# Kernel optimization log

Measured on AMD Instinct MI355X. Metric: run time of the kernel, lower is better.

## Reference

```python
import jax, jax.numpy as jnp
import numpy as np

N_IN = 50000
N_OUT = 50000
DEG = 16
E = N_OUT * DEG
C = 64
F = 64


def cartesian_to_spherical(cart, extents):
    # cart: [E,3]
    r_plane_2 = cart[..., 0] ** 2 + cart[..., 1] ** 2
    r_2 = r_plane_2 + cart[..., 2] ** 2
    r_safe = jnp.maximum(jnp.sqrt(r_2), 1e-10)
    cos_phi = cart[..., 2] / r_safe
    r_plane_safe = jnp.maximum(jnp.sqrt(r_plane_2), 1e-10)
    sin_theta = cart[..., 1] / r_plane_safe
    cos_theta = cart[..., 0] / r_plane_safe
    r_normalized = r_safe / extents
    return jnp.stack([r_normalized, cos_phi, sin_theta, cos_theta], axis=-1)  # [E,4]


def setup_inputs() -> dict:
    key = jax.random.key(0)
    k1, k2, k3, k4, k5 = jax.random.split(key, 5)
    input_features = jax.random.normal(k1, (N_IN, C), dtype=jnp.float32)
    input_positions = jax.random.uniform(k2, (N_IN, 3), dtype=jnp.float32)
    output_positions = jax.random.uniform(k3, (N_OUT, 3), dtype=jnp.float32)
    extents = jnp.ones((1,), dtype=jnp.float32)
    kernel = jax.random.normal(k4, (4, C, F), dtype=jnp.float32) * (1.0 / np.sqrt(C))
    bias = jnp.zeros((F,), dtype=jnp.float32)
    neighbors_index = jax.random.randint(k5, (E,), 0, N_IN, dtype=jnp.int32)
    neighbors_row_splits = (DEG * jnp.arange(N_OUT + 1)).astype(jnp.int32)
    return {
        "input_features": input_features,
        "input_positions": input_positions,
        "output_positions": output_positions,
        "extents": extents,
        "kernel": kernel,
        "bias": bias,
        "neighbors_index": neighbors_index,
        "neighbors_row_splits": neighbors_row_splits,
    }


def reference(input_features, input_positions, output_positions, extents,
              kernel, bias, neighbors_index, neighbors_row_splits):
    n_out = output_positions.shape[0]
    n_edges = neighbors_index.shape[0]
    counts = neighbors_row_splits[1:] - neighbors_row_splits[:-1]  # [N_out]
    # segment id of each edge (which output point it belongs to)
    seg_ids = jnp.repeat(jnp.arange(n_out), counts, total_repeat_length=n_edges)
    expanded_query = output_positions[seg_ids]                     # [E,3]
    difference = input_positions[neighbors_index] - expanded_query  # [E,3]
    sph = cartesian_to_spherical(difference, extents)              # [E,4]
    neighbors_feats = input_features[neighbors_index]              # [E,C]
    # contract features with kernel over C first -> [E,4,F] (avoids [E,C,F])
    tmp = jnp.einsum('ec,scf->esf', neighbors_feats, kernel)
    out_edge = jnp.einsum('es,esf->ef', sph, tmp)                  # [E,F]
    out_features = jax.ops.segment_sum(out_edge, seg_ids, num_segments=n_out)
    out_features = out_features + bias
    return out_features
```

## Files before the change

kernel.cpp:

```cpp
#include <hip/hip_runtime.h>

typedef unsigned short u16;
typedef __attribute__((ext_vector_type(8))) short bf16x8;
typedef __attribute__((ext_vector_type(4))) float f32x4;

#define WPB   4
#define BLOCK (WPB * 64)

__device__ __forceinline__ u16 f2bf(float f) {
    union { float f; unsigned u; } v; v.f = f;
    unsigned r = v.u + 0x7fff + ((v.u >> 16) & 1);
    return (u16)(r >> 16);
}

__global__ __launch_bounds__(BLOCK, 3)
void sphconv_mfma(const float* __restrict__ feats,
                  const float* __restrict__ in_pos,
                  const float* __restrict__ out_pos,
                  const float* __restrict__ extents,
                  const float* __restrict__ kmat,
                  const float* __restrict__ bias,
                  const int* __restrict__ nidx,
                  const int* __restrict__ rsplits,
                  float* __restrict__ out,
                  int n_out, int ntiles)
{
    __shared__ u16 KB[4 * 8 * 64 * 8];
    __shared__ int   idxL[WPB][16][16];
    __shared__ float sphL[WPB][16][16][4];

    const int tid  = threadIdx.x;
    const int wave = tid >> 6;
    const int lane = tid & 63;

    for (int i = tid; i < 16384; i += BLOCK) {
        const int n = i & 63, k = i >> 6;
        const int kstep = k >> 5, quad = (k >> 3) & 3, j = k & 7;
        const int ntile = n >> 4, lanep = (quad << 4) | (n & 15);
        KB[((((ntile << 3) | kstep) << 6) | lanep) * 8 + j] = f2bf(kmat[i]);
    }
    __syncthreads();

    const int tile = blockIdx.x * WPB + wave;
    if (tile >= ntiles) return;

    const float inv_ext = __fdividef(1.0f, extents[0]);

    #pragma unroll
    for (int u = 0; u < 4; ++u) {
        const int slot = (u << 6) | lane;
        const int m = slot >> 4, t = slot & 15;
        const int o = (tile << 4) | m;
        float rn = 0.f, cph = 0.f, sth = 0.f, cth = 0.f;
        int idx = 0;
        if (o < n_out) {
            const int e0 = rsplits[o], e1 = rsplits[o + 1];
            const int e = e0 + t;
            if (e < e1) {
                idx = nidx[e];
                const float dx = in_pos[idx * 3 + 0] - out_pos[o * 3 + 0];
                const float dy = in_pos[idx * 3 + 1] - out_pos[o * 3 + 1];
                const float dz = in_pos[idx * 3 + 2] - out_pos[o * 3 + 2];
                const float rp2 = dx * dx + dy * dy;
                const float r2  = rp2 + dz * dz;
                const float rs  = fmaxf(sqrtf(r2), 1e-10f);
                const float rp  = fmaxf(sqrtf(rp2), 1e-10f);
                const float ir  = __fdividef(1.0f, rs);
                const float irp = __fdividef(1.0f, rp);
                rn  = rs * inv_ext;
                cph = dz * ir;
                sth = dy * irp;
                cth = dx * irp;
            }
        }
        idxL[wave][t][m] = idx;
        f32x4 sv; sv.x = rn; sv.y = cph; sv.z = sth; sv.w = cth;
        *(f32x4*)&sphL[wave][t][m][0] = sv;
    }
    __builtin_amdgcn_wave_barrier();

    const int m    = lane & 15;
    const int quad = lane >> 4;
    float acc[8][8];
    #pragma unroll
    for (int ks = 0; ks < 8; ++ks)
        #pragma unroll
        for (int j = 0; j < 8; ++j) acc[ks][j] = 0.f;

    #pragma unroll 4
    for (int t = 0; t < 16; ++t) {
        const int   idx = idxL[wave][t][m];
        const f32x4 sv  = *(const f32x4*)&sphL[wave][t][m][0];
        const float* fr = feats + (idx << 6) + (quad << 3);
        const float4 lo0 = *(const float4*)(fr +  0);
        const float4 lo1 = *(const float4*)(fr +  4);
        const float4 hi0 = *(const float4*)(fr + 32);
        const float4 hi1 = *(const float4*)(fr + 36);
        #pragma unroll
        for (int s = 0; s < 4; ++s) {
            const float w = sv[s];
            float* aL = acc[2 * s];
            float* aH = acc[2 * s + 1];
            aL[0] = fmaf(w, lo0.x, aL[0]); aL[1] = fmaf(w, lo0.y, aL[1]);
            aL[2] = fmaf(w, lo0.z, aL[2]); aL[3] = fmaf(w, lo0.w, aL[3]);
            aL[4] = fmaf(w, lo1.x, aL[4]); aL[5] = fmaf(w, lo1.y, aL[5]);
            aL[6] = fmaf(w, lo1.z, aL[6]); aL[7] = fmaf(w, lo1.w, aL[7]);
            aH[0] = fmaf(w, hi0.x, aH[0]); aH[1] = fmaf(w, hi0.y, aH[1]);
            aH[2] = fmaf(w, hi0.z, aH[2]); aH[3] = fmaf(w, hi0.w, aH[3]);
            aH[4] = fmaf(w, hi1.x, aH[4]); aH[5] = fmaf(w, hi1.y, aH[5]);
            aH[6] = fmaf(w, hi1.z, aH[6]); aH[7] = fmaf(w, hi1.w, aH[7]);
        }
    }

    bf16x8 afr[8];
    #pragma unroll
    for (int ks = 0; ks < 8; ++ks) {
        union { u16 h[8]; bf16x8 v; } p;
        #pragma unroll
        for (int j = 0; j < 8; ++j) p.h[j] = f2bf(acc[ks][j]);
        afr[ks] = p.v;
    }

    const int obase = tile << 4;
    #pragma unroll
    for (int nt = 0; nt < 4; ++nt) {
        f32x4 C = {0.f, 0.f, 0.f, 0.f};
        const u16* kb = &KB[((nt << 3) << 6) * 8 + lane * 8];
        #pragma unroll
        for (int ks = 0; ks < 8; ++ks) {
            const bf16x8 b = *(const bf16x8*)(kb + (ks << 6) * 8);
            C = __builtin_amdgcn_mfma_f32_16x16x32_bf16(afr[ks], b, C, 0, 0, 0);
        }
        const int f  = (nt << 4) | m;
        const float bv = bias[f];
        #pragma unroll
        for (int r = 0; r < 4; ++r) {
            const int oo = obase + (quad << 2) + r;
            if (oo < n_out) out[(oo << 6) | f] = C[r] + bv;
        }
    }
}

extern "C" void kernel_launch(void* const* d_in, const int* in_sizes, int n_in,
                              void* d_out, int out_size, void* d_ws, size_t ws_size,
                              hipStream_t stream) {
    const float* feats   = (const float*)d_in[0];
    const float* in_pos  = (const float*)d_in[1];
    const float* out_pos = (const float*)d_in[2];
    const float* extents = (const float*)d_in[3];
    const float* kmat    = (const float*)d_in[4];
    const float* bias    = (const float*)d_in[5];
    const int*   nidx    = (const int*)d_in[6];
    const int*   rsplits = (const int*)d_in[7];
    const int n_out  = in_sizes[7] - 1;
    const int ntiles = (n_out + 15) >> 4;
    const int grid   = (ntiles + WPB - 1) / WPB;

    sphconv_mfma<<<grid, BLOCK, 0, stream>>>(
        feats, in_pos, out_pos, extents, kmat, bias, nidx, rsplits,
        (float*)d_out, n_out, ntiles);
}
```

Before: 128.3 us.

## Pre-convert features to bf16 in workspace and restructure gather with shuffles

Adds a prep kernel that converts the input features to bf16 and pre-swizzles the weight matrix into a workspace buffer. The main kernel then gathers half-size feature rows and copies the pre-swizzled weights instead of converting them per block. Spherical coordinates and neighbor indices now move through wave shuffles instead of LDS, and the channel dimension is processed in two halves to cut register pressure. The extra prep pass reads and writes the whole feature array each call and lowers the precision of the gathered features; a path without bf16 conversion is kept for when the workspace is too small.

```diff
diff --git a/kernel.cpp b/kernel.cpp
--- a/kernel.cpp
+++ b/kernel.cpp
@@ -2,141 +2,173 @@
 
 typedef unsigned short u16;
 typedef __attribute__((ext_vector_type(8))) short bf16x8;
+typedef __attribute__((ext_vector_type(8))) unsigned short u16x8;
 typedef __attribute__((ext_vector_type(4))) float f32x4;
 
 #define WPB   4
 #define BLOCK (WPB * 64)
 
+__device__ __forceinline__ float bf2f(u16 u) {
+    union { unsigned i; float f; } v; v.i = (unsigned)u << 16; return v.f;
+}
 __device__ __forceinline__ u16 f2bf(float f) {
     union { float f; unsigned u; } v; v.f = f;
     unsigned r = v.u + 0x7fff + ((v.u >> 16) & 1);
     return (u16)(r >> 16);
 }
 
+__global__ __launch_bounds__(256)
+void prep_kernel(const float* __restrict__ feats, const float* __restrict__ kmat,
+                 u16* __restrict__ fbf, u16* __restrict__ kbg, int nfeat8) {
+    const int id = blockIdx.x * 256 + threadIdx.x;
+    if (id < nfeat8) {
+        const float4 a = ((const float4*)feats)[2 * id];
+        const float4 b = ((const float4*)feats)[2 * id + 1];
+        union { u16 h[8]; int4 v; } p;
+        p.h[0] = f2bf(a.x); p.h[1] = f2bf(a.y); p.h[2] = f2bf(a.z); p.h[3] = f2bf(a.w);
+        p.h[4] = f2bf(b.x); p.h[5] = f2bf(b.y); p.h[6] = f2bf(b.z); p.h[7] = f2bf(b.w);
+        ((int4*)fbf)[id] = p.v;
+    }
+    if (id < 16384) {
+        const int k = id >> 6, n = id & 63;
+        const int nt = n >> 4, ks = k >> 5;
+        const int lanep = (((k >> 3) & 3) << 4) | (n & 15), j = k & 7;
+        kbg[(((((nt << 3) | ks) << 6) | lanep) << 3) | j] = f2bf(kmat[id]);
+    }
+}
+
+template<bool USE_WS>
 __global__ __launch_bounds__(BLOCK, 3)
-void sphconv_mfma(const float* __restrict__ feats,
-                  const float* __restrict__ in_pos,
-                  const float* __restrict__ out_pos,
-                  const float* __restrict__ extents,
-                  const float* __restrict__ kmat,
-                  const float* __restrict__ bias,
-                  const int* __restrict__ nidx,
-                  const int* __restrict__ rsplits,
-                  float* __restrict__ out,
-                  int n_out, int ntiles)
+void sphconv_main(const float* __restrict__ featsf, const u16* __restrict__ fbf,
+                  const float* __restrict__ in_pos, const float* __restrict__ out_pos,
+                  const float* __restrict__ extents, const float* __restrict__ kmat,
+                  const u16* __restrict__ kbg, const float* __restrict__ bias,
+                  const int* __restrict__ nidx, const int* __restrict__ rsplits,
+                  float* __restrict__ out, int n_out, int ntiles, int n_edges)
 {
-    __shared__ u16 KB[4 * 8 * 64 * 8];
-    __shared__ int   idxL[WPB][16][16];
-    __shared__ float sphL[WPB][16][16][4];
-
-    const int tid  = threadIdx.x;
-    const int wave = tid >> 6;
-    const int lane = tid & 63;
-
-    for (int i = tid; i < 16384; i += BLOCK) {
-        const int n = i & 63, k = i >> 6;
-        const int kstep = k >> 5, quad = (k >> 3) & 3, j = k & 7;
-        const int ntile = n >> 4, lanep = (quad << 4) | (n & 15);
-        KB[((((ntile << 3) | kstep) << 6) | lanep) * 8 + j] = f2bf(kmat[i]);
+    __shared__ u16 KB[16384];
+    const int tid = threadIdx.x, wave = tid >> 6, lane = tid & 63;
+
+    if constexpr (USE_WS) {
+        const int4* s = (const int4*)kbg; int4* d = (int4*)KB;
+        for (int i = tid; i < 2048; i += BLOCK) d[i] = s[i];
+    } else {
+        for (int i = tid; i < 16384; i += BLOCK) {
+            const int k = i >> 6, n = i & 63;
+            const int nt = n >> 4, ks = k >> 5;
+            const int lanep = (((k >> 3) & 3) << 4) | (n & 15), j = k & 7;
+            KB[(((((nt << 3) | ks) << 6) | lanep) << 3) | j] = f2bf(kmat[i]);
+        }
     }
     __syncthreads();
 
     const int tile = blockIdx.x * WPB + wave;
     if (tile >= ntiles) return;
 
-    const float inv_ext = __fdividef(1.0f, extents[0]);
-
+    const int m = lane & 15, quad = lane >> 4;
+    const int obase = tile << 4;
+    const int o  = obase + m;
+    const int oc = min(o, n_out - 1);
+    const int e0 = rsplits[oc];
+    const int e1 = rsplits[oc + 1];
+    const float qx = out_pos[oc * 3 + 0];
+    const float qy = out_pos[oc * 3 + 1];
+    const float qz = out_pos[oc * 3 + 2];
+    const float inv_ext = __fdividef(1.f, extents[0]);
+
+    float sph_r[4][4]; int idx_r[4];
     #pragma unroll
     for (int u = 0; u < 4; ++u) {
-        const int slot = (u << 6) | lane;
-        const int m = slot >> 4, t = slot & 15;
-        const int o = (tile << 4) | m;
-        float rn = 0.f, cph = 0.f, sth = 0.f, cth = 0.f;
-        int idx = 0;
-        if (o < n_out) {
-            const int e0 = rsplits[o], e1 = rsplits[o + 1];
-            const int e = e0 + t;
-            if (e < e1) {
-                idx = nidx[e];
-                const float dx = in_pos[idx * 3 + 0] - out_pos[o * 3 + 0];
-                const float dy = in_pos[idx * 3 + 1] - out_pos[o * 3 + 1];
-                const float dz = in_pos[idx * 3 + 2] - out_pos[o * 3 + 2];
-                const float rp2 = dx * dx + dy * dy;
-                const float r2  = rp2 + dz * dz;
-                const float rs  = fmaxf(sqrtf(r2), 1e-10f);
-                const float rp  = fmaxf(sqrtf(rp2), 1e-10f);
-                const float ir  = __fdividef(1.0f, rs);
-                const float irp = __fdividef(1.0f, rp);
-                rn  = rs * inv_ext;
-                cph = dz * ir;
-                sth = dy * irp;
-                cth = dx * irp;
+        const int t = (u << 2) | quad;
+        const int e = e0 + t;
+        const bool v = (o < n_out) && (e < e1);
+        const int id = nidx[min(e, n_edges - 1)];
+        const float dx = in_pos[id * 3 + 0] - qx;
+        const float dy = in_pos[id * 3 + 1] - qy;
+        const float dz = in_pos[id * 3 + 2] - qz;
+        const float rp2 = dx * dx + dy * dy;
+        const float r2  = rp2 + dz * dz;
+        const float rs  = fmaxf(sqrtf(r2), 1e-10f);
+        const float rp  = fmaxf(sqrtf(rp2), 1e-10f);
+        const float ir  = __fdividef(1.f, rs);
+        const float irp = __fdividef(1.f, rp);
+        sph_r[u][0] = v ? rs * inv_ext : 0.f;
+        sph_r[u][1] = v ? dz * ir      : 0.f;
+        sph_r[u][2] = v ? dy * irp     : 0.f;
+        sph_r[u][3] = v ? dx * irp     : 0.f;
+        idx_r[u] = id;
+    }
+
+    int idx_sh[16];
+    #pragma unroll
+    for (int t = 0; t < 16; ++t)
+        idx_sh[t] = __shfl(idx_r[t >> 2], ((t & 3) << 4) | m, 64);
+
+    f32x4 C[4] = {{0,0,0,0},{0,0,0,0},{0,0,0,0},{0,0,0,0}};
+    const bf16x8* kbp = (const bf16x8*)KB;
+
+    #pragma unroll
+    for (int h = 0; h < 2; ++h) {
+        float acc[4][8];
+        #pragma unroll
+        for (int s = 0; s < 4; ++s)
+            #pragma unroll
+            for (int j = 0; j < 8; ++j) acc[s][j] = 0.f;
+
+        #pragma unroll
+        for (int t = 0; t < 16; ++t) {
+            const int src = ((t & 3) << 4) | m;
+            float fv[8];
+            if constexpr (USE_WS) {
+                const u16x8 fr = *(const u16x8*)(fbf + (idx_sh[t] << 6) + (h << 5) + (quad << 3));
+                #pragma unroll
+                for (int j = 0; j < 8; ++j) fv[j] = bf2f(fr[j]);
+            } else {
+                const float* fp = featsf + (idx_sh[t] << 6) + (h << 5) + (quad << 3);
+                const float4 A0 = *(const float4*)fp;
+                const float4 A1 = *(const float4*)(fp + 4);
+                fv[0] = A0.x; fv[1] = A0.y; fv[2] = A0.z; fv[3] = A0.w;
+                fv[4] = A1.x; fv[5] = A1.y; fv[6] = A1.z; fv[7] = A1.w;
             }
-        }
-        idxL[wave][t][m] = idx;
-        f32x4 sv; sv.x = rn; sv.y = cph; sv.z = sth; sv.w = cth;
-        *(f32x4*)&sphL[wave][t][m][0] = sv;
-    }
-    __builtin_amdgcn_wave_barrier();
-
-    const int m    = lane & 15;
-    const int quad = lane >> 4;
-    float acc[8][8];
-    #pragma unroll
-    for (int ks = 0; ks < 8; ++ks)
-        #pragma unroll
-        for (int j = 0; j < 8; ++j) acc[ks][j] = 0.f;
-
-    #pragma unroll 4
-    for (int t = 0; t < 16; ++t) {
-        const int   idx = idxL[wave][t][m];
-        const f32x4 sv  = *(const f32x4*)&sphL[wave][t][m][0];
-        const float* fr = feats + (idx << 6) + (quad << 3);
-        const float4 lo0 = *(const float4*)(fr +  0);
-        const float4 lo1 = *(const float4*)(fr +  4);
-        const float4 hi0 = *(const float4*)(fr + 32);
-        const float4 hi1 = *(const float4*)(fr + 36);
+            const float s0 = __shfl(sph_r[t >> 2][0], src, 64);
+            const float s1 = __shfl(sph_r[t >> 2][1], src, 64);
+            const float s2 = __shfl(sph_r[t >> 2][2], src, 64);
+            const float s3 = __shfl(sph_r[t >> 2][3], src, 64);
+            #pragma unroll
+            for (int j = 0; j < 8; ++j) {
+                acc[0][j] = fmaf(s0, fv[j], acc[0][j]);
+                acc[1][j] = fmaf(s1, fv[j], acc[1][j]);
+                acc[2][j] = fmaf(s2, fv[j], acc[2][j]);
+                acc[3][j] = fmaf(s3, fv[j], acc[3][j]);
+            }
+        }
+
+        bf16x8 afr[4];
         #pragma unroll
         for (int s = 0; s < 4; ++s) {
-            const float w = sv[s];
-            float* aL = acc[2 * s];
-            float* aH = acc[2 * s + 1];
-            aL[0] = fmaf(w, lo0.x, aL[0]); aL[1] = fmaf(w, lo0.y, aL[1]);
-            aL[2] = fmaf(w, lo0.z, aL[2]); aL[3] = fmaf(w, lo0.w, aL[3]);
-            aL[4] = fmaf(w, lo1.x, aL[4]); aL[5] = fmaf(w, lo1.y, aL[5]);
-            aL[6] = fmaf(w, lo1.z, aL[6]); aL[7] = fmaf(w, lo1.w, aL[7]);
-            aH[0] = fmaf(w, hi0.x, aH[0]); aH[1] = fmaf(w, hi0.y, aH[1]);
-            aH[2] = fmaf(w, hi0.z, aH[2]); aH[3] = fmaf(w, hi0.w, aH[3]);
-            aH[4] = fmaf(w, hi1.x, aH[4]); aH[5] = fmaf(w, hi1.y, aH[5]);
-            aH[6] = fmaf(w, hi1.z, aH[6]); aH[7] = fmaf(w, hi1.w, aH[7]);
-        }
-    }
-
-    bf16x8 afr[8];
-    #pragma unroll
-    for (int ks = 0; ks < 8; ++ks) {
-        union { u16 h[8]; bf16x8 v; } p;
-        #pragma unroll
-        for (int j = 0; j < 8; ++j) p.h[j] = f2bf(acc[ks][j]);
-        afr[ks] = p.v;
-    }
-
-    const int obase = tile << 4;
+            union { u16 hh[8]; bf16x8 v; } p;
+            #pragma unroll
+            for (int j = 0; j < 8; ++j) p.hh[j] = f2bf(acc[s][j]);
+            afr[s] = p.v;
+        }
+
+        #pragma unroll
+        for (int nt = 0; nt < 4; ++nt)
+            #pragma unroll
+            for (int s = 0; s < 4; ++s) {
+                const bf16x8 b = kbp[(((nt << 3) | ((s << 1) | h)) << 6) | lane];
+                C[nt] = __builtin_amdgcn_mfma_f32_16x16x32_bf16(afr[s], b, C[nt], 0, 0, 0);
+            }
+    }
+
     #pragma unroll
     for (int nt = 0; nt < 4; ++nt) {
-        f32x4 C = {0.f, 0.f, 0.f, 0.f};
-        const u16* kb = &KB[((nt << 3) << 6) * 8 + lane * 8];
-        #pragma unroll
-        for (int ks = 0; ks < 8; ++ks) {
-            const bf16x8 b = *(const bf16x8*)(kb + (ks << 6) * 8);
-            C = __builtin_amdgcn_mfma_f32_16x16x32_bf16(afr[ks], b, C, 0, 0, 0);
-        }
-        const int f  = (nt << 4) | m;
+        const int f = (nt << 4) | m;
         const float bv = bias[f];
         #pragma unroll
         for (int r = 0; r < 4; ++r) {
             const int oo = obase + (quad << 2) + r;
-            if (oo < n_out) out[(oo << 6) | f] = C[r] + bv;
+            if (oo < n_out) out[(oo << 6) | f] = C[nt][r] + bv;
         }
     }
 }
@@ -152,11 +184,27 @@
     const float* bias    = (const float*)d_in[5];
     const int*   nidx    = (const int*)d_in[6];
     const int*   rsplits = (const int*)d_in[7];
-    const int n_out  = in_sizes[7] - 1;
-    const int ntiles = (n_out + 15) >> 4;
-    const int grid   = (ntiles + WPB - 1) / WPB;
-
-    sphconv_mfma<<<grid, BLOCK, 0, stream>>>(
-        feats, in_pos, out_pos, extents, kmat, bias, nidx, rsplits,
-        (float*)d_out, n_out, ntiles);
-}
+    const int n_out   = in_sizes[7] - 1;
+    const int n_edges = in_sizes[6];
+    const int ntiles  = (n_out + 15) >> 4;
+    const int grid    = (ntiles + WPB - 1) / WPB;
+
+    const size_t fbf_bytes = (size_t)in_sizes[0] * 2;
+    const size_t need = fbf_bytes + 32768;
+
+    if (ws_size >= need) {
+        u16* fbf = (u16*)d_ws;
+        u16* kbg = (u16*)((char*)d_ws + fbf_bytes);
+        const int nfeat8 = in_sizes[0] / 8;
+        const int pmax   = nfeat8 > 16384 ? nfeat8 : 16384;
+        const int pgrid  = (pmax + 255) / 256;
+        prep_kernel<<<pgrid, 256, 0, stream>>>(feats, kmat, fbf, kbg, nfeat8);
+        sphconv_main<true><<<grid, BLOCK, 0, stream>>>(
+            feats, fbf, in_pos, out_pos, extents, kmat, kbg, bias,
+            nidx, rsplits, (float*)d_out, n_out, ntiles, n_edges);
+    } else {
+        sphconv_main<false><<<grid, BLOCK, 0, stream>>>(
+            feats, nullptr, in_pos, out_pos, extents, kmat, nullptr, bias,
+            nidx, rsplits, (float*)d_out, n_out, ntiles, n_edges);
+    }
+}
```

After: 151.2 us. 1.18x slower.
